# Kernel tuning notes

Measured on AMD Instinct MI355X. Metric: run time of the kernel, lower is better.

## Reference

```python
import jax, jax.numpy as jnp
import numpy as np

T, B, I, H = 129, 1024, 512, 2048


def setup_inputs() -> dict:
    key = jax.random.key(0)
    ks = jax.random.split(key, 12)
    s = 1.0 / np.sqrt(H)  # torch RNNCell/Linear default U(-1/sqrt(H), 1/sqrt(H))

    def u(k, shape):
        return jax.random.uniform(k, shape, jnp.float32, -s, s)

    x = jax.random.normal(ks[0], (T, B, I), jnp.float32)
    return {
        "x": x,
        "enc_Wih": u(ks[1], (H, I)), "enc_Whh": u(ks[2], (H, H)),
        "enc_bih": u(ks[3], (H,)),   "enc_bhh": u(ks[4], (H,)),
        "dec_Wih": u(ks[5], (H, I)), "dec_Whh": u(ks[6], (H, H)),
        "dec_bih": u(ks[7], (H,)),   "dec_bhh": u(ks[8], (H,)),
        "ro_W": u(ks[9], (I, H)),    "ro_b": u(ks[10], (I,)),
    }


def reference(x, enc_Wih, enc_Whh, enc_bih, enc_bhh,
              dec_Wih, dec_Whh, dec_bih, dec_bhh, ro_W, ro_b):
    T_, B_, I_ = x.shape
    H_ = enc_Whh.shape[0]
    k = (T_ - 3) // 2

    # ---- encode: k+2 RNNCell steps over x[0:k+2] ----
    def enc_step(h, xt):
        h = jnp.tanh(xt @ enc_Wih.T + enc_bih + h @ enc_Whh.T + enc_bhh)
        return h, None

    h0 = jnp.zeros((B_, H_), x.dtype)
    h, _ = jax.lax.scan(enc_step, h0, x[:k + 2])

    # begin_char: one-hot at index 0 (also the default fill of `outputs`)
    begin = jnp.zeros((B_, I_), x.dtype).at[:, 0].set(1.0)

    # ---- decode: k+1 steps, input is zeros (so zeros @ dec_Wih == 0) ----
    def dec_step(carry, _):
        h, done = carry
        h = jnp.tanh(dec_bih + h @ dec_Whh.T + dec_bhh)
        out = jax.nn.log_softmax(h @ ro_W.T + ro_b, axis=1)  # [B, I]
        z = (jnp.argmax(out, axis=1) == 2).astype(x.dtype)
        done = jnp.maximum(done, z)
        b = done[:, None]
        o = (1.0 - b) * out + b * begin
        return (h, done), o

    done0 = jnp.zeros((B_,), x.dtype)
    (_, _), outputs = jax.lax.scan(dec_step, (h, done0), None, length=k + 1)
    return outputs  # [k+1, B, I]
```

## Files before the change

### kernel.cpp

```cpp
#include <hip/hip_runtime.h>
#include <math.h>

constexpr int Bsz  = 1024;
constexpr int Isz  = 512;
constexpr int Hsz  = 2048;
constexpr int Tenc = 65;
constexpr int Tdec = 64;
constexpr int BI   = Bsz * Isz;
constexpr int MNh  = Bsz * Hsz;

typedef _Float16 half8 __attribute__((ext_vector_type(8)));
typedef float    f32x4 __attribute__((ext_vector_type(4)));
typedef unsigned int uint;
typedef unsigned short ushort;

__device__ inline uint pack_split(float v) {
    _Float16 a0 = (_Float16)v;
    float r = (v - (float)a0) * 4096.f;
    _Float16 a1 = (_Float16)r;
    return ((uint)__builtin_bit_cast(ushort, a1) << 16) | __builtin_bit_cast(ushort, a0);
}

struct U8 { uint4 a, b; };
__device__ inline U8 ld8(const uint* __restrict__ p) {
    U8 r; r.a = *(const uint4*)p; r.b = *(const uint4*)(p + 4); return r;
}

__device__ inline void split8(const U8& v, half8& lo, half8& hi) {
    union { uint4 u; float f[4]; } A, B;
    A.u = v.a; B.u = v.b;
    float x[8] = {A.f[0], A.f[1], A.f[2], A.f[3], B.f[0], B.f[1], B.f[2], B.f[3]};
#pragma unroll
    for (int e = 0; e < 8; ++e) {
        _Float16 a0 = (_Float16)x[e];
        float r = (x[e] - (float)a0) * 4096.f;
        lo[e] = a0; hi[e] = (_Float16)r;
    }
}

__device__ inline void unpack8(const U8& v, half8& lo, half8& hi) {
    union { uint u[4]; half8 h; } L, H;
    uint w[8] = {v.a.x, v.a.y, v.a.z, v.a.w, v.b.x, v.b.y, v.b.z, v.b.w};
#pragma unroll
    for (int q = 0; q < 4; ++q) {
        L.u[q] = __builtin_amdgcn_perm(w[2*q+1], w[2*q], 0x05040100u);
        H.u[q] = __builtin_amdgcn_perm(w[2*q+1], w[2*q], 0x07060302u);
    }
    lo = L.h; hi = H.h;
}

__device__ __forceinline__ void gll16(const uint* g, uint* l) {
    __builtin_amdgcn_global_load_lds(
        (const __attribute__((address_space(1))) void*)(uintptr_t)g,
        (__attribute__((address_space(3))) void*)(unsigned int)(uintptr_t)l,
        16, 0, 0);
}

__global__ __launch_bounds__(256, 2) void gemm_pk4(
    const uint* __restrict__ A1, int K1, const uint* __restrict__ B1,
    const uint* __restrict__ A2, int K2, const uint* __restrict__ B2,
    float* __restrict__ P, int M, int N, int GM, int GN, int KS)
{
    constexpr int NV = 8;
    __shared__ uint ldsA[2 * 4096];
    __shared__ uint ldsB[2 * 4096];

    const int tid  = threadIdx.x;
    const int wid  = tid >> 6, lane = tid & 63;
    const int wr   = wid >> 1, wc = wid & 1;
    const int kq   = lane >> 4, lr = lane & 15;

    const int L = blockIdx.x, xcd = L & 7, g = L >> 3;
    int n_b, m_b, ks;
    const int spx = GN >> 3;
    if (spx > 0) {
        n_b = xcd * spx + (g % spx);
        int r = g / spx; m_b = r % GM; ks = r / GM;
    } else {
        const int xpn = 8 / GN;
        n_b = xcd / xpn;
        int r = g * xpn + (xcd % xpn); m_b = r % GM; ks = r / GM;
    }
    const int m0 = m_b * 128, n0 = n_b * 128;

    int offA1[4], offA2[4], offB1[4], offB2[4];
#pragma unroll
    for (int q = 0; q < 4; ++q) {
        int U = q * 256 + tid, row = U >> 3, us = U & 7;
        int u = us ^ (row & 7);
        offA1[q] = (m0 + row) * K1 + u * 4;
        offA2[q] = (m0 + row) * K2 + u * 4;
        offB1[q] = (n0 + row) * K1 + u * 4;
        offB2[q] = (n0 + row) * K2 + u * 4;
    }
    const int ldsbase = wid * 256;

    const int R1 = K1 / 32;
    const int R  = (K1 + K2) / 32;
    const int nr = R / KS;
    const int r0 = ks * nr;

    auto STAGE = [&](int r, int bi) {
        uint* Ab = ldsA + bi * 4096;
        uint* Bb = ldsB + bi * 4096;
        const bool ph1 = r < R1;
        const int kl = (ph1 ? r : r - R1) * 32;
        const uint* As = ph1 ? A1 : A2;
        const uint* Bs = ph1 ? B1 : B2;
#pragma unroll
        for (int q = 0; q < 4; ++q)
            gll16(As + (ph1 ? offA1[q] : offA2[q]) + kl, Ab + q * 1024 + ldsbase);
#pragma unroll
        for (int q = 0; q < 4; ++q)
            gll16(Bs + (ph1 ? offB1[q] : offB2[q]) + kl, Bb + q * 1024 + ldsbase);
    };

    f32x4 acc0[4][4] = {}; f32x4 acc1[4][4] = {};

    auto FRAG = [&](const uint* buf, int row, half8& lo, half8& hi) {
        const int b = row * 8, s = row & 7;
        U8 v;
        v.a = *(const uint4*)(buf + (b + ((2 * kq)     ^ s)) * 4);
        v.b = *(const uint4*)(buf + (b + ((2 * kq + 1) ^ s)) * 4);
        unpack8(v, lo, hi);
    };

    auto COMPUTE = [&](int bi) {
        const uint* Ab = ldsA + bi * 4096;
        const uint* Bb = ldsB + bi * 4096;
        half8 a0[4], a1[4];
#pragma unroll
        for (int i = 0; i < 4; ++i) FRAG(Ab, wr * 64 + i * 16 + lr, a0[i], a1[i]);
#pragma unroll
        for (int j = 0; j < 4; ++j) {
            half8 b0, b1;
            FRAG(Bb, wc * 64 + j * 16 + lr, b0, b1);
#pragma unroll
            for (int i = 0; i < 4; ++i) {
                acc0[i][j] = __builtin_amdgcn_mfma_f32_16x16x32_f16(a0[i], b0, acc0[i][j], 0, 0, 0);
                acc1[i][j] = __builtin_amdgcn_mfma_f32_16x16x32_f16(a1[i], b0, acc1[i][j], 0, 0, 0);
                acc1[i][j] = __builtin_amdgcn_mfma_f32_16x16x32_f16(a0[i], b1, acc1[i][j], 0, 0, 0);
            }
        }
    };

    STAGE(r0, 0);
    if (nr > 1) STAGE(r0 + 1, 1);
    __builtin_amdgcn_sched_barrier(0);
    if (nr > 1) asm volatile("s_waitcnt vmcnt(%0)" :: "i"(NV) : "memory");
    else        asm volatile("s_waitcnt vmcnt(0)"  ::: "memory");
    __builtin_amdgcn_s_barrier();
    __builtin_amdgcn_sched_barrier(0);

    int bi = 0;
    for (int t = 0; t < nr; ++t) {
        COMPUTE(bi);
        if (t + 1 < nr) {
            __builtin_amdgcn_sched_barrier(0);
            __builtin_amdgcn_s_barrier();
            __builtin_amdgcn_sched_barrier(0);
            if (t + 2 < nr) {
                STAGE(r0 + t + 2, bi);
                __builtin_amdgcn_sched_barrier(0);
                asm volatile("s_waitcnt vmcnt(%0)" :: "i"(NV) : "memory");
            } else {
                asm volatile("s_waitcnt vmcnt(0)" ::: "memory");
            }
            __builtin_amdgcn_s_barrier();
            __builtin_amdgcn_sched_barrier(0);
            bi ^= 1;
        }
    }

    float* Pk = P + (size_t)ks * M * N;
#pragma unroll
    for (int j = 0; j < 4; ++j) {
        const int n = n0 + wc * 64 + j * 16 + lr;
#pragma unroll
        for (int i = 0; i < 4; ++i) {
            const int mb = m0 + wr * 64 + i * 16 + kq * 4;
#pragma unroll
            for (int r = 0; r < 4; ++r)
                Pk[(size_t)(mb + r) * N + n] = acc0[i][j][r] + 0x1p-12f * acc1[i][j][r];
        }
    }
}

__global__ __launch_bounds__(256) void combine_h4(
    const float* __restrict__ P, const float* __restrict__ b1,
    const float* __restrict__ b2, uint* __restrict__ hout)
{
    const int i0 = (blockIdx.x * 256 + threadIdx.x) * 8;
    float s[8];
#pragma unroll
    for (int e = 0; e < 8; ++e) s[e] = 0.f;
#pragma unroll
    for (int p = 0; p < 4; ++p) {
        float4 a = *(const float4*)(P + (size_t)p * MNh + i0);
        float4 b = *(const float4*)(P + (size_t)p * MNh + i0 + 4);
        s[0] += a.x; s[1] += a.y; s[2] += a.z; s[3] += a.w;
        s[4] += b.x; s[5] += b.y; s[6] += b.z; s[7] += b.w;
    }
    const int n = i0 & (Hsz - 1);
    uint4 oa, ob;
    oa.x = pack_split(tanhf(s[0] + b1[n+0] + b2[n+0]));
    oa.y = pack_split(tanhf(s[1] + b1[n+1] + b2[n+1]));
    oa.z = pack_split(tanhf(s[2] + b1[n+2] + b2[n+2]));
    oa.w = pack_split(tanhf(s[3] + b1[n+3] + b2[n+3]));
    ob.x = pack_split(tanhf(s[4] + b1[n+4] + b2[n+4]));
    ob.y = pack_split(tanhf(s[5] + b1[n+5] + b2[n+5]));
    ob.z = pack_split(tanhf(s[6] + b1[n+6] + b2[n+6]));
    ob.w = pack_split(tanhf(s[7] + b1[n+7] + b2[n+7]));
    *(uint4*)(hout + i0)     = oa;
    *(uint4*)(hout + i0 + 4) = ob;
}

__global__ __launch_bounds__(256) void split_pack_k(
    const float* __restrict__ s, uint* __restrict__ d, int n)
{
    for (int i = blockIdx.x * 256 + threadIdx.x; i < n; i += gridDim.x * 256)
        d[i] = pack_split(s[i]);
}

template<int NPART>
__global__ __launch_bounds__(256) void logsoftmax_done(
    const float* __restrict__ parts, const float* __restrict__ rob,
    float* __restrict__ done, float* __restrict__ out)
{
    const int b   = blockIdx.x;
    const int tid = threadIdx.x;
    const size_t S = (size_t)BI;
    const float* row = parts + (size_t)b * Isz;

    float v0, v1;
    if (NPART == 1) { v0 = row[tid]; v1 = row[tid + 256]; }
    else {
        v0 = rob[tid]; v1 = rob[tid + 256];
#pragma unroll
        for (int p = 0; p < NPART; ++p) { v0 += row[p*S + tid]; v1 += row[p*S + tid + 256]; }
    }

    float mv; int mi;
    if (v0 >= v1) { mv = v0; mi = tid; } else { mv = v1; mi = tid + 256; }
#pragma unroll
    for (int off = 32; off; off >>= 1) {
        float ov = __shfl_xor(mv, off);
        int   oi = __shfl_xor(mi, off);
        if (ov > mv || (ov == mv && oi < mi)) { mv = ov; mi = oi; }
    }
    __shared__ float smv[4];
    __shared__ int   smi[4];
    __shared__ float sdone;
    const int wid = tid >> 6, lane = tid & 63;
    if (lane == 0) { smv[wid] = mv; smi[wid] = mi; }
    __syncthreads();
    if (tid == 0) {
        for (int w = 1; w < 4; ++w)
            if (smv[w] > smv[0] || (smv[w] == smv[0] && smi[w] < smi[0])) {
                smv[0] = smv[w]; smi[0] = smi[w];
            }
        float z = (smi[0] == 2) ? 1.f : 0.f;
        float dn = fmaxf(done[b], z);
        done[b] = dn;
        sdone = dn;
    }
    __syncthreads();
    mv = smv[0];

    float s = expf(v0 - mv) + expf(v1 - mv);
#pragma unroll
    for (int off = 32; off; off >>= 1) s += __shfl_xor(s, off);
    __shared__ float ssum[4];
    if (lane == 0) ssum[wid] = s;
    __syncthreads();
    if (tid == 0) ssum[0] = ssum[0] + ssum[1] + ssum[2] + ssum[3];
    __syncthreads();
    const float ls = logf(ssum[0]);

    float* orow = out + (size_t)b * Isz;
    if (sdone > 0.5f) {
        orow[tid]       = (tid == 0) ? 1.f : 0.f;
        orow[tid + 256] = 0.f;
    } else {
        orow[tid]       = v0 - mv - ls;
        orow[tid + 256] = v1 - mv - ls;
    }
}

#define SWZ(row, kk) (((row) * 4 + ((kk) ^ (((row) >> 1) & 3))) * 8)

template<int BM, int BN, int WR, int WC, int MP, int NP, bool TANH, bool PACKOUT>
__global__ __launch_bounds__(WR*WC*64) void gemm_sp(
    const float* __restrict__ A1, int K1, const void* __restrict__ B1,
    const uint*  __restrict__ A2, int K2, const void* __restrict__ B2,
    int b_f32,
    const float* __restrict__ bias1, const float* __restrict__ bias2,
    void* __restrict__ C, int M, int N)
{
    constexpr int NT  = WR * WC * 64;
    constexpr int AUP = BM * 4 / NT;
    constexpr int BUP = BN * 4 / NT;

    __shared__ __align__(16) _Float16 As0[BM*32], As1[BM*32];
    __shared__ __align__(16) _Float16 Bs0[BN*32], Bs1[BN*32];

    const int tid  = threadIdx.x;
    const int wid  = tid >> 6, lane = tid & 63;
    const int wrow = wid / WC, wcol = wid % WC;
    const int kq   = lane >> 4, lr = lane & 15;
    const int m0   = blockIdx.y * BM;
    const int n0   = blockIdx.x * BN;

    int aum[AUP], auk[AUP]; _Float16 *aw0[AUP], *aw1[AUP];
#pragma unroll
    for (int p = 0; p < AUP; ++p) {
        int u = tid + p * NT; aum[p] = u >> 2; auk[p] = u & 3;
        int o = SWZ(aum[p], auk[p]); aw0[p] = As0 + o; aw1[p] = As1 + o;
    }
    int bun[BUP], buk[BUP]; _Float16 *bw0[BUP], *bw1[BUP];
#pragma unroll
    for (int p = 0; p < BUP; ++p) {
        int u = tid + p * NT; bun[p] = u >> 2; buk[p] = u & 3;
        int o = SWZ(bun[p], buk[p]); bw0[p] = Bs0 + o; bw1[p] = Bs1 + o;
    }
    int aoff[MP], boff[NP];
#pragma unroll
    for (int i = 0; i < MP; ++i) { int m = wrow*(MP*16) + i*16 + lr; aoff[i] = SWZ(m, kq); }
#pragma unroll
    for (int j = 0; j < NP; ++j) { int n = wcol*(NP*16) + j*16 + lr; boff[j] = SWZ(n, kq); }

    f32x4 acc0[MP][NP] = {}; f32x4 acc1[MP][NP] = {};

    const int R = (K1 + K2) / 32;

    auto issue = [&](int rd, U8* aR, U8* bR) {
        const bool ph1 = (rd * 32) < K1;
        const int  kl  = ph1 ? rd * 32 : rd * 32 - K1;
        const int  Ka  = ph1 ? K1 : K2;
        const uint* Ap = ph1 ? (const uint*)A1 : A2;
        const uint* Bp = (const uint*)(ph1 ? B1 : B2);
#pragma unroll
        for (int p = 0; p < AUP; ++p)
            aR[p] = ld8(Ap + (size_t)(m0 + aum[p]) * Ka + kl + auk[p] * 8);
#pragma unroll
        for (int p = 0; p < BUP; ++p)
            bR[p] = ld8(Bp + (size_t)(n0 + bun[p]) * Ka + kl + buk[p] * 8);
    };

    auto stage = [&](U8* aR, U8* bR, bool aF32) {
#pragma unroll
        for (int p = 0; p < AUP; ++p) {
            half8 lo, hi;
            if (aF32) split8(aR[p], lo, hi); else unpack8(aR[p], lo, hi);
            *(half8*)aw0[p] = lo; *(half8*)aw1[p] = hi;
        }
#pragma unroll
        for (int p = 0; p < BUP; ++p) {
            half8 lo, hi;
            if (b_f32) split8(bR[p], lo, hi); else unpack8(bR[p], lo, hi);
            *(half8*)bw0[p] = lo; *(half8*)bw1[p] = hi;
        }
    };

    auto compute = [&]() {
        half8 a0[MP], a1[MP], b0[NP], b1[NP];
#pragma unroll
        for (int i = 0; i < MP; ++i) {
            a0[i] = *(const half8*)(As0 + aoff[i]);
            a1[i] = *(const half8*)(As1 + aoff[i]);
        }
#pragma unroll
        for (int j = 0; j < NP; ++j) {
            b0[j] = *(const half8*)(Bs0 + boff[j]);
            b1[j] = *(const half8*)(Bs1 + boff[j]);
        }
#pragma unroll
        for (int i = 0; i < MP; ++i)
#pragma unroll
            for (int j = 0; j < NP; ++j) {
                acc0[i][j] = __builtin_amdgcn_mfma_f32_16x16x32_f16(a0[i], b0[j], acc0[i][j], 0, 0, 0);
                acc1[i][j] = __builtin_amdgcn_mfma_f32_16x16x32_f16(a1[i], b0[j], acc1[i][j], 0, 0, 0);
                acc1[i][j] = __builtin_amdgcn_mfma_f32_16x16x32_f16(a0[i], b1[j], acc1[i][j], 0, 0, 0);
            }
    };

    U8 aA[AUP], bA[BUP], aB[AUP], bB[BUP];
    issue(0, aA, bA);
    for (int rd = 0; rd < R; rd += 2) {
        if (rd + 1 < R) issue(rd + 1, aB, bB);
        stage(aA, bA, (rd * 32) < K1);
        __syncthreads();
        compute();
        __syncthreads();
        if (rd + 1 < R) {
            if (rd + 2 < R) issue(rd + 2, aA, bA);
            stage(aB, bB, ((rd + 1) * 32) < K1);
            __syncthreads();
            compute();
            __syncthreads();
        }
    }

#pragma unroll
    for (int j = 0; j < NP; ++j) {
        const int n = n0 + wcol*(NP*16) + j*16 + lr;
        float bb = bias1 ? bias1[n] : 0.f;
        if (bias2) bb += bias2[n];
#pragma unroll
        for (int i = 0; i < MP; ++i) {
            const int mb = m0 + wrow*(MP*16) + i*16 + kq*4;
#pragma unroll
            for (int r = 0; r < 4; ++r) {
                float val = acc0[i][j][r] + 0x1p-12f * acc1[i][j][r] + bb;
                if (TANH) val = tanhf(val);
                if (PACKOUT)
                    ((uint*)C)[(size_t)(mb + r) * N + n] = pack_split(val);
                else
                    ((float*)C)[(size_t)(mb + r) * N + n] = val;
            }
        }
    }
}

extern "C" void kernel_launch(void* const* d_in, const int* in_sizes, int n_in,
                              void* d_out, int out_size, void* d_ws, size_t ws_size,
                              hipStream_t stream)
{
    const float* x    = (const float*)d_in[0];
    const float* eWih = (const float*)d_in[1];
    const float* eWhh = (const float*)d_in[2];
    const float* ebih = (const float*)d_in[3];
    const float* ebhh = (const float*)d_in[4];
    const float* dWhh = (const float*)d_in[6];
    const float* dbih = (const float*)d_in[7];
    const float* dbhh = (const float*)d_in[8];
    const float* roW  = (const float*)d_in[9];
    const float* rob  = (const float*)d_in[10];
    float* out = (float*)d_out;

    const size_t sz_pWih = (size_t)Hsz * Isz * 4;
    const size_t sz_pWhh = (size_t)Hsz * Hsz * 4;
    const size_t sz_proW = (size_t)Isz * Hsz * 4;
    const size_t sz_h    = (size_t)MNh * 4;
    const size_t sz_hp   = (size_t)4 * MNh * 4;
    const size_t sz_rp   = (size_t)16 * BI * 4;
    const size_t sz_done = (size_t)Bsz * 4;
    const size_t sz_px2  = (size_t)Tenc * BI * 4;
    const size_t sz_slot = (size_t)BI * 4;

    const size_t base = sz_pWih + 2*sz_pWhh + sz_proW + 2*sz_h + sz_hp + sz_rp + sz_done;
    const int mode = (ws_size >= base + sz_px2) ? 2
                   : (ws_size >= base + sz_slot) ? 1 : 0;

    char* ws = (char*)d_ws;

    if (mode >= 1) {
        size_t off = 0;
        uint* pWih   = (uint*)(ws + off); off += sz_pWih;
        uint* pWhh   = (uint*)(ws + off); off += sz_pWhh;
        uint* pdWhh  = (uint*)(ws + off); off += sz_pWhh;
        uint* proW   = (uint*)(ws + off); off += sz_proW;
        uint* hA     = (uint*)(ws + off); off += sz_h;
        uint* hB     = (uint*)(ws + off); off += sz_h;
        float* hparts= (float*)(ws + off); off += sz_hp;
        float* ropar = (float*)(ws + off); off += sz_rp;
        float* done  = (float*)(ws + off); off += sz_done;
        uint* px     = (uint*)(ws + off);

        split_pack_k<<<dim3(1024), dim3(256), 0, stream>>>(eWih, pWih,  Hsz*Isz);
        split_pack_k<<<dim3(2048), dim3(256), 0, stream>>>(eWhh, pWhh,  Hsz*Hsz);
        split_pack_k<<<dim3(2048), dim3(256), 0, stream>>>(dWhh, pdWhh, Hsz*Hsz);
        split_pack_k<<<dim3(1024), dim3(256), 0, stream>>>(roW,  proW,  Isz*Hsz);
        if (mode == 2)
            split_pack_k<<<dim3(2048), dim3(256), 0, stream>>>(x, px, Tenc*BI);

        hipMemsetAsync(hA,   0, sz_h,    stream);
        hipMemsetAsync(done, 0, sz_done, stream);

        uint* h[2] = { hA, hB };
        int cur = 0;
        for (int t = 0; t < Tenc; ++t) {
            const uint* xs;
            if (mode == 2) xs = px + (size_t)t * BI;
            else {
                split_pack_k<<<dim3(512), dim3(256), 0, stream>>>(
                    x + (size_t)t * BI, px, BI);
                xs = px;
            }
            gemm_pk4<<<dim3(512), dim3(256), 0, stream>>>(
                xs, Isz, pWih, h[cur], Hsz, pWhh,
                hparts, Bsz, Hsz, 8, 16, 4);
            combine_h4<<<dim3(1024), dim3(256), 0, stream>>>(
                hparts, ebih, ebhh, h[cur ^ 1]);
            cur ^= 1;
        }
        for (int t = 0; t < Tdec; ++t) {
            gemm_pk4<<<dim3(512), dim3(256), 0, stream>>>(
                nullptr, 0, nullptr, h[cur], Hsz, pdWhh,
                hparts, Bsz, Hsz, 8, 16, 4);
            combine_h4<<<dim3(1024), dim3(256), 0, stream>>>(
                hparts, dbih, dbhh, h[cur ^ 1]);
            cur ^= 1;
            gemm_pk4<<<dim3(512), dim3(256), 0, stream>>>(
                nullptr, 0, nullptr, h[cur], Hsz, proW,
                ropar, Bsz, Isz, 8, 4, 16);
            logsoftmax_done<16><<<dim3(Bsz), dim3(256), 0, stream>>>(
                ropar, rob, done, out + (size_t)t * BI);
        }
        return;
    }

    {
        const size_t sz_lg = (size_t)BI * 4;
        size_t off = 0;
        uint*  hA     = (uint*)(ws + off); off += sz_h;
        uint*  hB     = (uint*)(ws + off); off += sz_h;
        float* logits = (float*)(ws + off); off += sz_lg;
        float* done   = (float*)(ws + off);

        hipMemsetAsync(hA, 0, sz_h, stream);
        hipMemsetAsync(done, 0, sz_done, stream);

        uint* h[2] = { hA, hB };
        const dim3 blk(256);
        const dim3 grid_h(Hsz / 128, Bsz / 64);
        const dim3 grid_ro(Isz / 64, Bsz / 64);

        int cur = 0;
        for (int t = 0; t < Tenc; ++t) {
            gemm_sp<64, 128, 2, 2, 2, 4, true, true><<<grid_h, blk, 0, stream>>>(
                x + (size_t)t * BI, Isz, eWih,
                h[cur], Hsz, eWhh, 1,
                ebih, ebhh, h[cur ^ 1], Bsz, Hsz);
            cur ^= 1;
        }
        for (int t = 0; t < Tdec; ++t) {
            gemm_sp<64, 128, 2, 2, 2, 4, true, true><<<grid_h, blk, 0, stream>>>(
                nullptr, 0, nullptr, h[cur], Hsz, dWhh, 1,
                dbih, dbhh, h[cur ^ 1], Bsz, Hsz);
            cur ^= 1;
            gemm_sp<64, 64, 2, 2, 2, 2, false, false><<<grid_ro, blk, 0, stream>>>(
                nullptr, 0, nullptr, h[cur], Hsz, roW, 1,
                rob, nullptr, logits, Bsz, Isz);
            logsoftmax_done<1><<<dim3(Bsz), dim3(256), 0, stream>>>(
                logits, rob, done, out + (size_t)t * BI);
        }
    }
}
```

Before: 7.323 ms.

## Fuse decoder hidden and readout GEMMs into shared launches per step

Reorders the decoder so each step's readout GEMM and the next hidden-state GEMM both consume the same h and run in one combined kernel launch. The bias/tanh combine and the log-softmax/done update are likewise merged into one launch. The first decoder hidden step is hoisted before the loop, and the final step skips the unused hidden update. This halves launches per decode step and lets the two GEMMs fill the device together. The readout split-K is reduced from 16 to 8, adding per-block work for it.

Result: faster. 6.739 ms (-8.0%).

```diff
diff --git a/kernel.cpp b/kernel.cpp
--- a/kernel.cpp
+++ b/kernel.cpp
@@ -56,21 +56,19 @@
         16, 0, 0);
 }
 
-__global__ __launch_bounds__(256, 2) void gemm_pk4(
-    const uint* __restrict__ A1, int K1, const uint* __restrict__ B1,
-    const uint* __restrict__ A2, int K2, const uint* __restrict__ B2,
-    float* __restrict__ P, int M, int N, int GM, int GN, int KS)
+__device__ __forceinline__ void gemm_body(
+    uint* ldsA, uint* ldsB,
+    const uint* A1, int K1, const uint* B1,
+    const uint* A2, int K2, const uint* B2,
+    float* P, int M, int N, int GM, int GN, int KS, int bid)
 {
     constexpr int NV = 8;
-    __shared__ uint ldsA[2 * 4096];
-    __shared__ uint ldsB[2 * 4096];
-
     const int tid  = threadIdx.x;
     const int wid  = tid >> 6, lane = tid & 63;
     const int wr   = wid >> 1, wc = wid & 1;
     const int kq   = lane >> 4, lr = lane & 15;
 
-    const int L = blockIdx.x, xcd = L & 7, g = L >> 3;
+    const int xcd = bid & 7, g = bid >> 3;
     int n_b, m_b, ks;
     const int spx = GN >> 3;
     if (spx > 0) {
@@ -186,11 +184,39 @@
     }
 }
 
-__global__ __launch_bounds__(256) void combine_h4(
+__global__ __launch_bounds__(256, 2) void gemm_pk4(
+    const uint* __restrict__ A1, int K1, const uint* __restrict__ B1,
+    const uint* __restrict__ A2, int K2, const uint* __restrict__ B2,
+    float* __restrict__ P, int M, int N, int GM, int GN, int KS)
+{
+    __shared__ uint ldsA[2 * 4096];
+    __shared__ uint ldsB[2 * 4096];
+    gemm_body(ldsA, ldsB, A1, K1, B1, A2, K2, B2, P, M, N, GM, GN, KS, blockIdx.x);
+}
+
+__global__ __launch_bounds__(256, 2) void dec_work(
+    const uint* __restrict__ hcur, const uint* __restrict__ pdWhh,
+    const uint* __restrict__ proW,
+    float* __restrict__ hparts, float* __restrict__ ropar, int doH)
+{
+    __shared__ uint ldsA[2 * 4096];
+    __shared__ uint ldsB[2 * 4096];
+    const int bid = blockIdx.x;
+    if (bid < 512) {
+        if (!doH) return;
+        gemm_body(ldsA, ldsB, nullptr, 0, nullptr, hcur, Hsz, pdWhh,
+                  hparts, Bsz, Hsz, 8, 16, 4, bid);
+    } else {
+        gemm_body(ldsA, ldsB, nullptr, 0, nullptr, hcur, Hsz, proW,
+                  ropar, Bsz, Isz, 8, 4, 8, bid - 512);
+    }
+}
+
+__device__ __forceinline__ void combine_dev(
     const float* __restrict__ P, const float* __restrict__ b1,
-    const float* __restrict__ b2, uint* __restrict__ hout)
-{
-    const int i0 = (blockIdx.x * 256 + threadIdx.x) * 8;
+    const float* __restrict__ b2, uint* __restrict__ hout, int cb)
+{
+    const int i0 = (cb * 256 + threadIdx.x) * 8;
     float s[8];
 #pragma unroll
     for (int e = 0; e < 8; ++e) s[e] = 0.f;
@@ -215,19 +241,18 @@
     *(uint4*)(hout + i0 + 4) = ob;
 }
 
-__global__ __launch_bounds__(256) void split_pack_k(
-    const float* __restrict__ s, uint* __restrict__ d, int n)
-{
-    for (int i = blockIdx.x * 256 + threadIdx.x; i < n; i += gridDim.x * 256)
-        d[i] = pack_split(s[i]);
+__global__ __launch_bounds__(256) void combine_h4(
+    const float* __restrict__ P, const float* __restrict__ b1,
+    const float* __restrict__ b2, uint* __restrict__ hout)
+{
+    combine_dev(P, b1, b2, hout, blockIdx.x);
 }
 
 template<int NPART>
-__global__ __launch_bounds__(256) void logsoftmax_done(
+__device__ __forceinline__ void softmax_dev(
     const float* __restrict__ parts, const float* __restrict__ rob,
-    float* __restrict__ done, float* __restrict__ out)
-{
-    const int b   = blockIdx.x;
+    float* __restrict__ done, float* __restrict__ out, int b)
+{
     const int tid = threadIdx.x;
     const size_t S = (size_t)BI;
     const float* row = parts + (size_t)b * Isz;
@@ -287,6 +312,34 @@
     }
 }
 
+__global__ __launch_bounds__(256) void dec_fin(
+    const float* __restrict__ hparts, const float* __restrict__ dbih,
+    const float* __restrict__ dbhh, uint* __restrict__ hout,
+    const float* __restrict__ ropar, const float* __restrict__ rob,
+    float* __restrict__ done, float* __restrict__ out, int doH)
+{
+    const int bid = blockIdx.x;
+    if (bid < 1024) {
+        if (doH) combine_dev(hparts, dbih, dbhh, hout, bid);
+    } else {
+        softmax_dev<8>(ropar, rob, done, out, bid - 1024);
+    }
+}
+
+__global__ __launch_bounds__(256) void logsoftmax_done1(
+    const float* __restrict__ logits, const float* __restrict__ rob,
+    float* __restrict__ done, float* __restrict__ out)
+{
+    softmax_dev<1>(logits, rob, done, out, blockIdx.x);
+}
+
+__global__ __launch_bounds__(256) void split_pack_k(
+    const float* __restrict__ s, uint* __restrict__ d, int n)
+{
+    for (int i = blockIdx.x * 256 + threadIdx.x; i < n; i += gridDim.x * 256)
+        d[i] = pack_split(s[i]);
+}
+
 #define SWZ(row, kk) (((row) * 4 + ((kk) ^ (((row) >> 1) & 3))) * 8)
 
 template<int BM, int BN, int WR, int WC, int MP, int NP, bool TANH, bool PACKOUT>
@@ -443,7 +496,7 @@
     const size_t sz_proW = (size_t)Isz * Hsz * 4;
     const size_t sz_h    = (size_t)MNh * 4;
     const size_t sz_hp   = (size_t)4 * MNh * 4;
-    const size_t sz_rp   = (size_t)16 * BI * 4;
+    const size_t sz_rp   = (size_t)8 * BI * 4;
     const size_t sz_done = (size_t)Bsz * 4;
     const size_t sz_px2  = (size_t)Tenc * BI * 4;
     const size_t sz_slot = (size_t)BI * 4;
@@ -494,18 +547,20 @@
                 hparts, ebih, ebhh, h[cur ^ 1]);
             cur ^= 1;
         }
+        gemm_pk4<<<dim3(512), dim3(256), 0, stream>>>(
+            nullptr, 0, nullptr, h[cur], Hsz, pdWhh,
+            hparts, Bsz, Hsz, 8, 16, 4);
+        combine_h4<<<dim3(1024), dim3(256), 0, stream>>>(
+            hparts, dbih, dbhh, h[cur ^ 1]);
+        cur ^= 1;
         for (int t = 0; t < Tdec; ++t) {
-            gemm_pk4<<<dim3(512), dim3(256), 0, stream>>>(
-                nullptr, 0, nullptr, h[cur], Hsz, pdWhh,
-                hparts, Bsz, Hsz, 8, 16, 4);
-            combine_h4<<<dim3(1024), dim3(256), 0, stream>>>(
-                hparts, dbih, dbhh, h[cur ^ 1]);
+            const int doH = (t + 1 < Tdec) ? 1 : 0;
+            dec_work<<<dim3(768), dim3(256), 0, stream>>>(
+                h[cur], pdWhh, proW, hparts, ropar, doH);
+            dec_fin<<<dim3(2048), dim3(256), 0, stream>>>(
+                hparts, dbih, dbhh, h[cur ^ 1],
+                ropar, rob, done, out + (size_t)t * BI, doH);
             cur ^= 1;
-            gemm_pk4<<<dim3(512), dim3(256), 0, stream>>>(
-                nullptr, 0, nullptr, h[cur], Hsz, proW,
-                ropar, Bsz, Isz, 8, 4, 16);
-            logsoftmax_done<16><<<dim3(Bsz), dim3(256), 0, stream>>>(
-                ropar, rob, done, out + (size_t)t * BI);
         }
         return;
     }
@@ -542,7 +597,7 @@
             gemm_sp<64, 64, 2, 2, 2, 2, false, false><<<grid_ro, blk, 0, stream>>>(
                 nullptr, 0, nullptr, h[cur], Hsz, roW, 1,
                 rob, nullptr, logits, Bsz, Isz);
-            logsoftmax_done<1><<<dim3(Bsz), dim3(256), 0, stream>>>(
+            logsoftmax_done1<<<dim3(Bsz), dim3(256), 0, stream>>>(
                 logits, rob, done, out + (size_t)t * BI);
         }
     }
```
